# Kernel tuning notes

Hardware: AMD Instinct MI355X
Metric: run time of the kernel (lower is better)

## Reference

```python
import jax, jax.numpy as jnp
import numpy as np
from jax import lax

IN, H1, H2, F1, OUT = 26, 64, 32, 16, 10
B, T = 512, 1000


def _lstm(x, w_ih, w_hh, b_ih, b_hh):
    """PyTorch-convention LSTM (gate order i,f,g,o). x: [B,T,I].
    Returns (all hidden states [B,T,H], final hidden [B,H])."""
    Bx = x.shape[0]
    H = w_hh.shape[1]
    # Precompute input projections for all timesteps: [B,T,4H]
    xg = jnp.einsum('bti,gi->btg', x, w_ih) + b_ih + b_hh

    def step(carry, xg_t):
        h, c = carry
        gates = xg_t + h @ w_hh.T  # [B,4H]
        i, f, g, o = jnp.split(gates, 4, axis=-1)
        i = jax.nn.sigmoid(i)
        f = jax.nn.sigmoid(f)
        g = jnp.tanh(g)
        o = jax.nn.sigmoid(o)
        c = f * c + i * g
        h = o * jnp.tanh(c)
        return (h, c), h

    init = (jnp.zeros((Bx, H), x.dtype), jnp.zeros((Bx, H), x.dtype))
    (h_last, _), hs = lax.scan(step, init, xg.transpose(1, 0, 2))
    return hs.transpose(1, 0, 2), h_last


def setup_inputs() -> dict:
    key = jax.random.key(0)
    ks = jax.random.split(key, 14)

    def u(k, shape, fan):
        bound = 1.0 / np.sqrt(fan)
        return jax.random.uniform(k, shape, jnp.float32, -bound, bound)

    return {
        'x': jax.random.normal(ks[0], (B, 1, IN, T), jnp.float32),
        'w_ih1': u(ks[1], (4 * H1, IN), H1),
        'w_hh1': u(ks[2], (4 * H1, H1), H1),
        'b_ih1': u(ks[3], (4 * H1,), H1),
        'b_hh1': u(ks[4], (4 * H1,), H1),
        'w_ih2': u(ks[5], (4 * H2, H1), H2),
        'w_hh2': u(ks[6], (4 * H2, H2), H2),
        'b_ih2': u(ks[7], (4 * H2,), H2),
        'b_hh2': u(ks[8], (4 * H2,), H2),
        'w_fc1': u(ks[9], (F1, H2), H2),
        'b_fc1': u(ks[10], (F1,), H2),
        'w_fc2': u(ks[11], (OUT, F1), F1),
        'b_fc2': u(ks[12], (OUT,), F1),
    }


def reference(x, w_ih1, w_hh1, b_ih1, b_hh1, w_ih2, w_hh2, b_ih2, b_hh2,
              w_fc1, b_fc1, w_fc2, b_fc2):
    # [B,1,26,T] -> [B,26,T] -> [B,T,26]
    x = jnp.transpose(x[:, 0], (0, 2, 1))
    out1, _ = _lstm(x, w_ih1, w_hh1, b_ih1, b_hh1)
    # Dropout is identity in eval mode.
    _, h2 = _lstm(out1, w_ih2, w_hh2, b_ih2, b_hh2)  # final hidden [B,32]
    h = jax.nn.relu(h2 @ w_fc1.T + b_fc1)
    return h @ w_fc2.T + b_fc2  # [B,10]
```

## Files before the change

kernel.cpp:

```cpp
#include <hip/hip_runtime.h>
#include <hip/hip_bf16.h>


typedef __hip_bfloat16 bf16;
typedef _Float16 f16;
typedef _Float16 f16x8 __attribute__((ext_vector_type(8)));
typedef _Float16 f16x4 __attribute__((ext_vector_type(4)));
typedef float    f32x4 __attribute__((ext_vector_type(4)));

#define T_STEPS 1000
#define IN_DIM  26
#define EPB     16
#define CH      16
#define H1P     72
#define H2P     40
#define XP      40

#define NL2E  -1.4426950408889634f
#define N2L2E -2.8853900817779268f

__device__ __forceinline__ float bits2f(unsigned short h) {
    return __uint_as_float(((unsigned int)h) << 16);
}
__device__ __forceinline__ float ldv(const void* p, long i, bool isb) {
    return isb ? bits2f(((const unsigned short*)p)[i]) : ((const float*)p)[i];
}
__device__ __forceinline__ float rcp_(float x) { return __builtin_amdgcn_rcpf(x); }
__device__ __forceinline__ float ex2_(float x) { return __builtin_amdgcn_exp2f(x); }

__device__ __forceinline__ float lstm_act(float yi, float yf, float yg,
                                          float yo, float& c) {
    const float A  = ex2_(yi), F = ex2_(yf), B = ex2_(yg), O = ex2_(yo);
    const float a1 = 1.f + A, f1 = 1.f + F, b1 = 1.f + B, o1 = 1.f + O;
    const float ig = (2.f - b1) * rcp_(a1 * b1);
    c = fmaf(rcp_(f1), c, ig);
    const float C2  = ex2_(N2L2E * c);
    const float c1p = 1.f + C2;
    return (2.f - c1p) * rcp_(o1 * c1p);
}

#define MFMA(a, b, c) __builtin_amdgcn_mfma_f32_16x16x32_f16((a), (b), (c), 0, 0, 0)

__global__
__attribute__((amdgpu_flat_work_group_size(1024, 1024), amdgpu_waves_per_eu(4, 4)))
void lstm_fused(const void* __restrict__ x,
                const void* __restrict__ w_ih1, const void* __restrict__ w_hh1,
                const void* __restrict__ b_ih1, const void* __restrict__ b_hh1,
                const void* __restrict__ w_ih2, const void* __restrict__ w_hh2,
                const void* __restrict__ b_ih2, const void* __restrict__ b_hh2,
                const void* __restrict__ w_fc1, const void* __restrict__ b_fc1,
                const void* __restrict__ w_fc2, const void* __restrict__ b_fc2,
                void* __restrict__ out)
{
    const int tid  = threadIdx.x;
    const int lane = tid & 63;
    const int wv   = tid >> 6;
    const int ecol = lane & 15;
    const int g4   = lane >> 4;
    const int r15  = lane & 15;
    const int e0   = blockIdx.x * EPB;

    __shared__ __align__(16) f16    Xst[2][CH][EPB][XP];
    __shared__ __align__(16) f16    H1T[2][EPB][H1P];
    __shared__ __align__(16) f16    H2T[2][EPB][H2P];
    __shared__ __align__(16) float4 XG[2][1024];
    __shared__ __align__(16) float  f1s[EPB][16];

    bool isb = true;
    {
        const unsigned short* wu = (const unsigned short*)w_ih1;
        for (int k = 0; k < 64; ++k) {
            float v = fabsf(bits2f(wu[k]));
            if (!(v <= 0.1251f)) isb = false;
        }
    }

    {
        float4 z; z.x = z.y = z.z = z.w = 0.f;
        float4* p = (float4*)&Xst[0][0][0][0];
        for (int k = tid; k < (int)(sizeof(Xst) / 16); k += 1024) p[k] = z;
        float4* q = (float4*)&H1T[0][0][0];
        for (int k = tid; k < (int)(sizeof(H1T) / 16); k += 1024) q[k] = z;
        float4* r = (float4*)&H2T[0][0][0];
        for (int k = tid; k < (int)(sizeof(H2T) / 16); k += 1024) r[k] = z;
    }

    f16x8 W8[8]; f16x8 W4[4]; f32x4 C4[4];
    const int rr4 = wv & 3;
    if (wv < 4) {
#pragma unroll
        for (int gi = 0; gi < 4; ++gi) {
            const float sc = (gi == 2) ? N2L2E : NL2E;
            const int R = gi * 64 + 16 * rr4 + r15;
#pragma unroll
            for (int k0 = 0; k0 < 2; ++k0)
#pragma unroll
                for (int jj = 0; jj < 8; ++jj)
                    W8[gi * 2 + k0][jj] =
                        (f16)(sc * ldv(w_hh1, R * 64 + k0 * 32 + g4 * 8 + jj, isb));
        }
    } else if (wv < 8) {
#pragma unroll
        for (int gi = 0; gi < 4; ++gi) {
            const float sc = (gi == 2) ? N2L2E : NL2E;
            const int R = gi * 64 + 16 * rr4 + r15;
#pragma unroll
            for (int jj = 0; jj < 8; ++jj) {
                const int k = g4 * 8 + jj;
                W4[gi][jj] =
                    (f16)(k < IN_DIM ? sc * ldv(w_ih1, R * IN_DIM + k, isb) : 0.f);
            }
#pragma unroll
            for (int jj = 0; jj < 4; ++jj) {
                const int Rc = gi * 64 + 16 * rr4 + g4 * 4 + jj;
                C4[gi][jj] = sc * (ldv(b_ih1, Rc, isb) + ldv(b_hh1, Rc, isb));
            }
        }
    } else if (wv < 10) {
        const int hf = wv & 1;
#pragma unroll
        for (int gi = 0; gi < 4; ++gi) {
            const float sc = (gi == 2) ? N2L2E : NL2E;
            const int R = gi * 32 + 16 * hf + r15;
#pragma unroll
            for (int k0 = 0; k0 < 2; ++k0)
#pragma unroll
                for (int jj = 0; jj < 8; ++jj)
                    W8[gi * 2 + k0][jj] =
                        (f16)(sc * ldv(w_ih2, R * 64 + k0 * 32 + g4 * 8 + jj, isb));
#pragma unroll
            for (int jj = 0; jj < 8; ++jj)
                W4[gi][jj] = (f16)(sc * ldv(w_hh2, R * 32 + g4 * 8 + jj, isb));
#pragma unroll
            for (int jj = 0; jj < 4; ++jj) {
                const int Rc = gi * 32 + 16 * hf + g4 * 4 + jj;
                C4[gi][jj] = sc * (ldv(b_ih2, Rc, isb) + ldv(b_hh2, Rc, isb));
            }
        }
    }

    __syncthreads();

    auto stageRow = [&](int p, int c) {
        const int t0 = c * CH;
        const int nt = (T_STEPS - t0 < CH) ? (T_STEPS - t0) : CH;
        const int e = p / IN_DIM, i = p - e * IN_DIM;
        const long gb = ((long)(e0 + e) * IN_DIM + i) * T_STEPS + t0;
        float4 fb[4];
        if (isb) {
            const float4* q = (const float4*)((const unsigned short*)x + gb);
            fb[0] = q[0]; if (nt > 8) fb[1] = q[1];
        } else {
            const float4* q = (const float4*)((const float*)x + gb);
            fb[0] = q[0]; fb[1] = q[1];
            if (nt > 8) { fb[2] = q[2]; fb[3] = q[3]; }
        }
#pragma unroll
        for (int t = 0; t < CH; ++t) if (t < nt) {
            float v;
            if (isb) {
                unsigned int u =
                    __builtin_bit_cast(unsigned int, fb[t >> 3][(t >> 1) & 3]);
                v = bits2f((t & 1) ? (unsigned short)(u >> 16)
                                   : (unsigned short)(u & 0xffffu));
            } else {
                v = fb[t >> 2][t & 3];
            }
            Xst[c & 1][t][e][i] = (f16)v;
        }
    };

    if (tid < EPB * IN_DIM) stageRow(tid, 0);
    __syncthreads();

    if (wv >= 4 && wv < 8) {
        const f16x8 xf = *(const f16x8*)&Xst[0][0][ecol][g4 * 8];
#pragma unroll
        for (int gi = 0; gi < 4; ++gi) {
            f32x4 v = MFMA(W4[gi], xf, C4[gi]);
            *(f32x4*)&XG[0][((rr4 * 4 + gi) * 4 + g4) * 16 + ecol] = v;
        }
    }
    __syncthreads();

    if (wv < 4 || wv == 8 || wv == 9) __builtin_amdgcn_s_setprio(1);

    float cst[4] = {0.f, 0.f, 0.f, 0.f};

    for (int s = 0; s <= T_STEPS; ++s) {
        const int pc = s & 1, pp = pc ^ 1;

        if (wv < 4) {
            if (s < T_STEPS) {
                const f16x8 h1f0 = *(const f16x8*)&H1T[pp][ecol][g4 * 8];
                const f16x8 h1f1 = *(const f16x8*)&H1T[pp][ecol][32 + g4 * 8];
                f32x4 gt[4];
#pragma unroll
                for (int gi = 0; gi < 4; ++gi) {
                    const f32x4 xgc =
                        *(const f32x4*)&XG[pc][((rr4 * 4 + gi) * 4 + g4) * 16 + ecol];
                    f32x4 t0 = MFMA(W8[gi * 2 + 0], h1f0, xgc);
                    gt[gi]   = MFMA(W8[gi * 2 + 1], h1f1, t0);
                }
                f16x4 hh;
#pragma unroll
                for (int jj = 0; jj < 4; ++jj)
                    hh[jj] = (f16)lstm_act(gt[0][jj], gt[1][jj],
                                           gt[2][jj], gt[3][jj], cst[jj]);
                *(f16x4*)&H1T[pc][ecol][16 * rr4 + g4 * 4] = hh;
            }
        } else if (wv < 8) {
            if (s + 1 < T_STEPS) {
                const int sn = s + 1;
                const f16x8 xf =
                    *(const f16x8*)&Xst[(sn >> 4) & 1][sn & 15][ecol][g4 * 8];
#pragma unroll
                for (int gi = 0; gi < 4; ++gi) {
                    f32x4 v = MFMA(W4[gi], xf, C4[gi]);
                    *(f32x4*)&XG[pp][((rr4 * 4 + gi) * 4 + g4) * 16 + ecol] = v;
                }
            }
        } else if (wv < 10) {
            if (s >= 1) {
                const int hf = wv & 1;
                const f16x8 h1f0 = *(const f16x8*)&H1T[pp][ecol][g4 * 8];
                const f16x8 h1f1 = *(const f16x8*)&H1T[pp][ecol][32 + g4 * 8];
                const f16x8 h2f  = *(const f16x8*)&H2T[pc][ecol][g4 * 8];
                f32x4 gt[4];
#pragma unroll
                for (int gi = 0; gi < 4; ++gi) {
                    f32x4 t0 = MFMA(W8[gi * 2 + 0], h1f0, C4[gi]);
                    t0       = MFMA(W8[gi * 2 + 1], h1f1, t0);
                    gt[gi]   = MFMA(W4[gi], h2f, t0);
                }
                f16x4 hh;
#pragma unroll
                for (int jj = 0; jj < 4; ++jj)
                    hh[jj] = (f16)lstm_act(gt[0][jj], gt[1][jj],
                                           gt[2][jj], gt[3][jj], cst[jj]);
                *(f16x4*)&H2T[pp][ecol][16 * hf + g4 * 4] = hh;
            }
        } else {
            if ((s & (CH - 1)) == 0 && s + CH < T_STEPS) {
                const int c = (s >> 4) + 1;
                const int p = tid - 640;
                stageRow(p, c);
                if (p < EPB * IN_DIM - 384) stageRow(p + 384, c);
            }
        }

        __syncthreads();
    }

    if (tid < EPB * 16) {
        const int e = tid >> 4, o = tid & 15;
        float ss = ldv(b_fc1, o, isb);
#pragma unroll 8
        for (int k = 0; k < 32; ++k)
            ss = fmaf(ldv(w_fc1, o * 32 + k, isb), (float)H2T[1][e][k], ss);
        f1s[e][o] = fmaxf(ss, 0.f);
    }
    __syncthreads();
    if (tid < EPB * 10) {
        const int e = tid / 10, o = tid - e * 10;
        float ss = ldv(b_fc2, o, isb);
#pragma unroll
        for (int k = 0; k < 16; ++k)
            ss = fmaf(ldv(w_fc2, o * 16 + k, isb), f1s[e][k], ss);
        const long oi = (long)(e0 + e) * 10 + o;
        if (isb) ((bf16*)out)[oi] = __float2bfloat16(ss);
        else     ((float*)out)[oi] = ss;
    }
}

extern "C" void kernel_launch(void* const* d_in, const int* in_sizes, int n_in,
                              void* d_out, int out_size, void* d_ws, size_t ws_size,
                              hipStream_t stream) {
    lstm_fused<<<dim3(512 / EPB), dim3(1024), 0, stream>>>(
        d_in[0], d_in[1], d_in[2], d_in[3], d_in[4],
        d_in[5], d_in[6], d_in[7], d_in[8],
        d_in[9], d_in[10], d_in[11], d_in[12], d_out);
}
```

Baseline: 825.8 us.

## Merge input-projection waves into layer-1 waves and spread x staging over steps

```diff
diff --git a/kernel.cpp b/kernel.cpp
--- a/kernel.cpp
+++ b/kernel.cpp
@@ -12,6 +12,7 @@
 #define IN_DIM  26
 #define EPB     16
 #define CH      16
+#define NCHUNK  62
 #define H1P     72
 #define H2P     40
 #define XP      40
@@ -42,7 +43,7 @@
 #define MFMA(a, b, c) __builtin_amdgcn_mfma_f32_16x16x32_f16((a), (b), (c), 0, 0, 0)
 
 __global__
-__attribute__((amdgpu_flat_work_group_size(1024, 1024), amdgpu_waves_per_eu(4, 4)))
+__attribute__((amdgpu_flat_work_group_size(512, 512), amdgpu_waves_per_eu(2, 2)))
 void lstm_fused(const void* __restrict__ x,
                 const void* __restrict__ w_ih1, const void* __restrict__ w_hh1,
                 const void* __restrict__ b_ih1, const void* __restrict__ b_hh1,
@@ -60,11 +61,10 @@
     const int r15  = lane & 15;
     const int e0   = blockIdx.x * EPB;
 
-    __shared__ __align__(16) f16    Xst[2][CH][EPB][XP];
-    __shared__ __align__(16) f16    H1T[2][EPB][H1P];
-    __shared__ __align__(16) f16    H2T[2][EPB][H2P];
-    __shared__ __align__(16) float4 XG[2][1024];
-    __shared__ __align__(16) float  f1s[EPB][16];
+    __shared__ __align__(16) f16   Xst[2][CH][EPB][XP];
+    __shared__ __align__(16) f16   H1T[2][EPB][H1P];
+    __shared__ __align__(16) f16   H2T[2][EPB][H2P];
+    __shared__ __align__(16) float f1s[EPB][16];
 
     bool isb = true;
     {
@@ -78,32 +78,25 @@
     {
         float4 z; z.x = z.y = z.z = z.w = 0.f;
         float4* p = (float4*)&Xst[0][0][0][0];
-        for (int k = tid; k < (int)(sizeof(Xst) / 16); k += 1024) p[k] = z;
+        for (int k = tid; k < (int)(sizeof(Xst) / 16); k += 512) p[k] = z;
         float4* q = (float4*)&H1T[0][0][0];
-        for (int k = tid; k < (int)(sizeof(H1T) / 16); k += 1024) q[k] = z;
+        for (int k = tid; k < (int)(sizeof(H1T) / 16); k += 512) q[k] = z;
         float4* r = (float4*)&H2T[0][0][0];
-        for (int k = tid; k < (int)(sizeof(H2T) / 16); k += 1024) r[k] = z;
+        for (int k = tid; k < (int)(sizeof(H2T) / 16); k += 512) r[k] = z;
     }
 
     f16x8 W8[8]; f16x8 W4[4]; f32x4 C4[4];
-    const int rr4 = wv & 3;
     if (wv < 4) {
 #pragma unroll
         for (int gi = 0; gi < 4; ++gi) {
             const float sc = (gi == 2) ? N2L2E : NL2E;
-            const int R = gi * 64 + 16 * rr4 + r15;
+            const int R = gi * 64 + 16 * wv + r15;
 #pragma unroll
             for (int k0 = 0; k0 < 2; ++k0)
 #pragma unroll
                 for (int jj = 0; jj < 8; ++jj)
                     W8[gi * 2 + k0][jj] =
                         (f16)(sc * ldv(w_hh1, R * 64 + k0 * 32 + g4 * 8 + jj, isb));
-        }
-    } else if (wv < 8) {
-#pragma unroll
-        for (int gi = 0; gi < 4; ++gi) {
-            const float sc = (gi == 2) ? N2L2E : NL2E;
-            const int R = gi * 64 + 16 * rr4 + r15;
 #pragma unroll
             for (int jj = 0; jj < 8; ++jj) {
                 const int k = g4 * 8 + jj;
@@ -112,12 +105,12 @@
             }
 #pragma unroll
             for (int jj = 0; jj < 4; ++jj) {
-                const int Rc = gi * 64 + 16 * rr4 + g4 * 4 + jj;
+                const int Rc = gi * 64 + 16 * wv + g4 * 4 + jj;
                 C4[gi][jj] = sc * (ldv(b_ih1, Rc, isb) + ldv(b_hh1, Rc, isb));
             }
         }
-    } else if (wv < 10) {
-        const int hf = wv & 1;
+    } else if (wv < 6) {
+        const int hf = wv - 4;
 #pragma unroll
         for (int gi = 0; gi < 4; ++gi) {
             const float sc = (gi == 2) ? N2L2E : NL2E;
@@ -171,19 +164,17 @@
     };
 
     if (tid < EPB * IN_DIM) stageRow(tid, 0);
+    if (tid >= 448 && tid < 448 + 26) stageRow(tid - 448, 1);
     __syncthreads();
 
-    if (wv >= 4 && wv < 8) {
+    f32x4 xgc[4];
+    if (wv < 4) {
         const f16x8 xf = *(const f16x8*)&Xst[0][0][ecol][g4 * 8];
 #pragma unroll
-        for (int gi = 0; gi < 4; ++gi) {
-            f32x4 v = MFMA(W4[gi], xf, C4[gi]);
-            *(f32x4*)&XG[0][((rr4 * 4 + gi) * 4 + g4) * 16 + ecol] = v;
-        }
-    }
-    __syncthreads();
-
-    if (wv < 4 || wv == 8 || wv == 9) __builtin_amdgcn_s_setprio(1);
+        for (int gi = 0; gi < 4; ++gi) xgc[gi] = MFMA(W4[gi], xf, C4[gi]);
+    }
+
+    if (wv < 6) __builtin_amdgcn_s_setprio(1);
 
     float cst[4] = {0.f, 0.f, 0.f, 0.f};
 
@@ -194,35 +185,38 @@
             if (s < T_STEPS) {
                 const f16x8 h1f0 = *(const f16x8*)&H1T[pp][ecol][g4 * 8];
                 const f16x8 h1f1 = *(const f16x8*)&H1T[pp][ecol][32 + g4 * 8];
+                const bool nx = (s + 1 < T_STEPS);
+                f16x8 xf = {};
+                if (nx) {
+                    const int sn = s + 1;
+                    xf = *(const f16x8*)&Xst[(sn >> 4) & 1][sn & 15][ecol][g4 * 8];
+                }
                 f32x4 gt[4];
 #pragma unroll
                 for (int gi = 0; gi < 4; ++gi) {
-                    const f32x4 xgc =
-                        *(const f32x4*)&XG[pc][((rr4 * 4 + gi) * 4 + g4) * 16 + ecol];
-                    f32x4 t0 = MFMA(W8[gi * 2 + 0], h1f0, xgc);
+                    f32x4 t0 = MFMA(W8[gi * 2 + 0], h1f0, xgc[gi]);
                     gt[gi]   = MFMA(W8[gi * 2 + 1], h1f1, t0);
+                }
+                f32x4 xgn[4];
+                if (nx) {
+#pragma unroll
+                    for (int gi = 0; gi < 4; ++gi)
+                        xgn[gi] = MFMA(W4[gi], xf, C4[gi]);
                 }
                 f16x4 hh;
 #pragma unroll
                 for (int jj = 0; jj < 4; ++jj)
                     hh[jj] = (f16)lstm_act(gt[0][jj], gt[1][jj],
                                            gt[2][jj], gt[3][jj], cst[jj]);
-                *(f16x4*)&H1T[pc][ecol][16 * rr4 + g4 * 4] = hh;
-            }
-        } else if (wv < 8) {
-            if (s + 1 < T_STEPS) {
-                const int sn = s + 1;
-                const f16x8 xf =
-                    *(const f16x8*)&Xst[(sn >> 4) & 1][sn & 15][ecol][g4 * 8];
-#pragma unroll
-                for (int gi = 0; gi < 4; ++gi) {
-                    f32x4 v = MFMA(W4[gi], xf, C4[gi]);
-                    *(f32x4*)&XG[pp][((rr4 * 4 + gi) * 4 + g4) * 16 + ecol] = v;
-                }
-            }
-        } else if (wv < 10) {
+                *(f16x4*)&H1T[pc][ecol][16 * wv + g4 * 4] = hh;
+                if (nx) {
+#pragma unroll
+                    for (int gi = 0; gi < 4; ++gi) xgc[gi] = xgn[gi];
+                }
+            }
+        } else if (wv < 6) {
             if (s >= 1) {
-                const int hf = wv & 1;
+                const int hf = wv - 4;
                 const f16x8 h1f0 = *(const f16x8*)&H1T[pp][ecol][g4 * 8];
                 const f16x8 h1f1 = *(const f16x8*)&H1T[pp][ecol][32 + g4 * 8];
                 const f16x8 h2f  = *(const f16x8*)&H2T[pc][ecol][g4 * 8];
@@ -241,11 +235,11 @@
                 *(f16x4*)&H2T[pp][ecol][16 * hf + g4 * 4] = hh;
             }
         } else {
-            if ((s & (CH - 1)) == 0 && s + CH < T_STEPS) {
-                const int c = (s >> 4) + 1;
-                const int p = tid - 640;
-                stageRow(p, c);
-                if (p < EPB * IN_DIM - 384) stageRow(p + 384, c);
+            const int s1 = s + 1, c = (s1 >> 4) + 1;
+            if (c <= NCHUNK) {
+                const int slice = s1 & 15;
+                const int p = slice * 26 + (wv - 6) * 13 + lane;
+                if (lane < 13) stageRow(p, c);
             }
         }
 
@@ -276,7 +270,7 @@
 extern "C" void kernel_launch(void* const* d_in, const int* in_sizes, int n_in,
                               void* d_out, int out_size, void* d_ws, size_t ws_size,
                               hipStream_t stream) {
-    lstm_fused<<<dim3(512 / EPB), dim3(1024), 0, stream>>>(
+    lstm_fused<<<dim3(512 / EPB), dim3(512), 0, stream>>>(
         d_in[0], d_in[1], d_in[2], d_in[3], d_in[4],
         d_in[5], d_in[6], d_in[7], d_in[8],
         d_in[9], d_in[10], d_in[11], d_in[12], d_out);
```

Measured after the change: 821.7 us. No clear change (-0.5%).
